# Optimization experiments

Hardware: AMD Instinct MI355X
Metric: run time of the kernel (lower is better)

## Reference

```python
import jax, jax.numpy as jnp
import numpy as np

ICM2IFS = 2.99792458e-05
KB = 0.6950389


def _forward(T, Er, cortim, dt, psi0, Hfull, W1, b1, W2, b2, W3, b3, W4, b4,
             save_interval, remat=False):
    # Faithful vectorized translation of MLNISE.forward with T_correction='ML',
    # explicitTemp='None', saveCoherence=False, saveU=False. The original
    # nested (ii, jj) Python loops are fully independent across (ii, jj), so
    # they are vectorized into one [B, N, N] pass per timestep.
    B, Tp1, N, _ = Hfull.shape
    kBT = T * KB                                             # [B]
    factor = (1j * 2.0 * np.pi * ICM2IFS) * dt.astype(jnp.complex64)  # [B]
    E0, C0 = jnp.linalg.eigh(Hfull[:, 0])
    phiB0 = jnp.einsum('bji,bjk->bik', C0.astype(jnp.complex64),
                       psi0.astype(jnp.complex64))           # Cold^T @ psi0
    jidx = jnp.arange(N)[None, :, None]

    def mlp(x):
        h = jax.nn.elu(x @ W1.T + b1)
        h = jax.nn.elu(h @ W2.T + b2)
        h = jax.nn.elu(h @ W3.T + b3)
        return jax.nn.elu(h @ W4.T + b4)

    def step(carry, Ht):
        Cold, Eold, phiB = carry
        E, C = jnp.linalg.eigh(Ht)
        S = jnp.einsum('bja,bjc->bac', C, Cold)              # S[b, jj, ii] = (C^T Cold)
        kk = jnp.argmax(S * S, axis=1)                       # [B, N] max over jj per ii
        is_kk = jidx == kk[:, None, :]                       # [B, N(jj), N(ii)]
        DE = jnp.where(is_kk, 0.0, E[:, :, None] - Eold[:, None, :])
        phi2 = jnp.real(phiB[:, :, 0]) ** 2 + jnp.imag(phiB[:, :, 0]) ** 2  # [B, N]
        p_ii = phi2[:, None, :]
        p_jj = phi2[:, :, None]
        m = p_ii > 0.01 * p_jj
        ratio = jnp.where(m, p_jj / jnp.where(m, p_ii, 1.0), 100.0)
        kbt = kBT[:, None, None]
        ones = jnp.ones_like(S)
        feat = jnp.stack([DE, ratio, S, kbt * ones,
                          Er[:, None, None] * ones, cortim[:, None, None] * ones,
                          jnp.zeros_like(S), jnp.exp(DE / kbt)], axis=-1)  # [B,N,N,8]
        corr = (mlp(feat.reshape(B * N * N, 8)) + 1.0).reshape(B, N, N)
        S2 = S * corr
        CD = jnp.sum(jnp.where(is_kk, 0.0, S2 * S2), axis=1)  # [B, N] per ii
        S_kk = jnp.take_along_axis(S2, kk[:, None, :], axis=1)[:, 0, :]  # [B, N]
        nrm = jnp.abs(S_kk)
        nrm = jnp.where(nrm > 0, nrm, 1.0)
        pos = (1.0 - CD) > 0
        newval = jnp.where(pos, jnp.sqrt(jnp.clip(1.0 - CD, 0.0)) * S_kk / nrm, S_kk)
        S2 = jnp.where(is_kk, newval[:, None, :], S2)
        phase = jnp.exp(-E.astype(jnp.complex64) * factor[:, None])  # [B, N]
        U = phase[:, :, None] * S2.astype(jnp.complex64)      # diag(phase) @ S
        phiB = U @ phiB
        phiB = phiB / jnp.sqrt(jnp.sum(jnp.real(phiB) ** 2 + jnp.imag(phiB) ** 2,
                                       axis=1, keepdims=True))
        ploc = jnp.einsum('bij,bjk->bik', C.astype(jnp.complex64), phiB)
        ps = jnp.real(ploc[:, :, 0]) ** 2 + jnp.imag(ploc[:, :, 0]) ** 2
        return (C, E, phiB), ps

    f = jax.checkpoint(step) if remat else step
    Hts = jnp.moveaxis(Hfull[:, 1:], 1, 0)                   # time-major [steps,B,N,N]
    _, ps_all = jax.lax.scan(f, (C0, E0, phiB0), Hts)
    saved = jnp.moveaxis(ps_all[save_interval - 1::save_interval], 0, 1)
    return jnp.concatenate([(psi0[:, :, 0] ** 2)[:, None, :], saved], axis=1)


def setup_inputs() -> dict:
    key = jax.random.key(0)
    ks = jax.random.split(key, 8)
    B, N, steps, SI = 32, 32, 600, 10
    A = 50.0 * jax.random.normal(ks[0], (B, steps + 1, N, N), dtype=jnp.float32)
    Hfull = 0.5 * (A + jnp.swapaxes(A, -1, -2))              # symmetric per snapshot
    psi0 = jnp.zeros((B, N, 1), jnp.float32).at[:, 0, 0].set(1.0)
    T = 250.0 + 100.0 * jax.random.uniform(ks[1], (B,), jnp.float32)
    Er = 1.0 + 35.0 * jax.random.uniform(ks[2], (B,), jnp.float32)
    cortim = 10.0 + 100.0 * jax.random.uniform(ks[3], (B,), jnp.float32)
    dt = jnp.ones((B,), jnp.float32)
    total_time = jnp.full((B,), float(steps), jnp.float32)
    reps = jnp.arange(B, dtype=jnp.int32)

    def lin(k, fo, fi):
        kw, kb = jax.random.split(k)
        bnd = 1.0 / np.sqrt(fi)
        W = jax.random.uniform(kw, (fo, fi), jnp.float32, -bnd, bnd) / 10.0
        b = jax.random.uniform(kb, (fo,), jnp.float32, -bnd, bnd)
        return W, b

    W1, b1 = lin(ks[4], 75, 8)
    W2, b2 = lin(ks[5], 75, 75)
    W3, b3 = lin(ks[6], 75, 75)
    W4, b4 = lin(ks[7], 1, 75)
    return dict(T=T, Er=Er, cortim=cortim, total_time=total_time, dt=dt, reps=reps,
                psi0=psi0, Hfull=Hfull, W1=W1, b1=b1, W2=W2, b2=b2, W3=W3, b3=b3,
                W4=W4, b4=b4, save_interval=SI)


def reference(T, Er, cortim, total_time, dt, reps, psi0, Hfull,
              W1, b1, W2, b2, W3, b3, W4, b4, save_interval):
    # total_time/dt only set the (static) number of steps = Hfull.shape[1]-1;
    # reps only sets the batch size. Both are encoded in the array shapes.
    return _forward(T, Er, cortim, dt, psi0, Hfull,
                    W1, b1, W2, b2, W3, b3, W4, b4, save_interval)
```

## Files before the change

kernel.cpp:

```cpp
#include <hip/hip_runtime.h>
#include <math.h>


#define NB 32
#define NN 32
#define NSTEPS 600
#define NT1 601
#define NSI 10
#define NH 75
#define NU 80
#define NKB 20
#define NIB 8
#define NG 16

#define ICM2IFS 2.99792458e-05
#define KBOLTZ 0.6950389f
#define TWO_PI 6.283185307179586476925286766559

__device__ __forceinline__ float elu1(float x) { return x > 0.f ? x : (__expf(x) - 1.f); }

__global__ __launch_bounds__(128) void eigh_kernel(const float* __restrict__ Hf,
                                                   float* __restrict__ E_all,
                                                   float* __restrict__ CT_all)
{
    __shared__ double A[NN][NN + 1];
    __shared__ float  V[NN][NN + 1];
    __shared__ double csC[16], csS[16];
    __shared__ int   prC[16], qrC[16];
    __shared__ double redv;
    __shared__ int   rankl[NN];

    const int idx = blockIdx.x;
    const int tid = threadIdx.x;
    const float* Hp = Hf + (size_t)idx * (NN * NN);

    for (int e = tid; e < NN * NN; e += 128) {
        A[e >> 5][e & 31] = (double)Hp[e];
        V[e >> 5][e & 31] = ((e >> 5) == (e & 31)) ? 1.f : 0.f;
    }
    __syncthreads();

    if (tid < 64) {
        double part = 0.0;
        for (int e = tid; e < NN * NN; e += 64) { double v = A[e >> 5][e & 31]; part += v * v; }
        #pragma unroll
        for (int off = 32; off > 0; off >>= 1) part += __shfl_down(part, off);
        if (tid == 0) redv = part;
    }
    __syncthreads();
    const double tol2 = 1e-16 * redv;

    for (int sweep = 0; sweep < 10; ++sweep) {
        for (int r = 0; r < NN - 1; ++r) {
            if (tid < 16) {
                int m = tid, p, q;
                if (m == 0) { p = 0; q = 1 + (r % 31); }
                else { p = 1 + ((m + r) % 31); q = 1 + ((31 - m + r) % 31); }
                double apq = A[p][q];
                double c = 1.0, sn = 0.0;
                if (apq != 0.0) {
                    double theta = 0.5 * (A[q][q] - A[p][p]) / apq;
                    double tt = 1.0 / (fabs(theta) + sqrt(theta * theta + 1.0));
                    if (theta < 0.0) tt = -tt;
                    c = 1.0 / sqrt(tt * tt + 1.0);
                    sn = tt * c;
                }
                csC[m] = c; csS[m] = sn; prC[m] = p; qrC[m] = q;
            }
            __syncthreads();
            #pragma unroll
            for (int it = 0; it < 4; ++it) {
                int task = tid + it * 128;
                int m = task >> 5, jc = task & 31;
                int p = prC[m], q = qrC[m];
                double c = csC[m], sn = csS[m];
                double ap = A[p][jc], aq = A[q][jc];
                A[p][jc] = c * ap - sn * aq;
                A[q][jc] = sn * ap + c * aq;
            }
            __syncthreads();
            #pragma unroll
            for (int it = 0; it < 8; ++it) {
                int task = tid + it * 128;
                int m = (task >> 5) & 15, ir = task & 31;
                int p = prC[m], q = qrC[m];
                if (task < 512) {
                    double c = csC[m], sn = csS[m];
                    double aip = A[ir][p], aiq = A[ir][q];
                    A[ir][p] = c * aip - sn * aiq;
                    A[ir][q] = sn * aip + c * aiq;
                } else {
                    float cf = (float)csC[m], sf = (float)csS[m];
                    float vip = V[ir][p], viq = V[ir][q];
                    V[ir][p] = cf * vip - sf * viq;
                    V[ir][q] = sf * vip + cf * viq;
                }
            }
            __syncthreads();
        }
        if (sweep >= 3) {
            if (tid < 64) {
                double o = 0.0;
                for (int e = tid; e < NN * NN; e += 64) {
                    int i2 = e >> 5, j2 = e & 31;
                    double v = A[i2][j2];
                    o += (i2 != j2) ? v * v : 0.0;
                }
                #pragma unroll
                for (int off = 32; off > 0; off >>= 1) o += __shfl_down(o, off);
                if (tid == 0) redv = o;
            }
            __syncthreads();
            if (redv <= tol2) break;
        }
    }
    __syncthreads();

    if (tid < NN) {
        double ei = A[tid][tid];
        int rk = 0;
        for (int j2 = 0; j2 < NN; ++j2) {
            double ej = A[j2][j2];
            rk += (ej < ei || (ej == ei && j2 < tid)) ? 1 : 0;
        }
        rankl[tid] = rk;
        E_all[(size_t)idx * NN + rk] = (float)ei;
    }
    __syncthreads();
    float* ct = CT_all + (size_t)idx * NN * NN;
    for (int e = tid; e < NN * NN; e += 128) {
        int col = e >> 5, m2 = e & 31;
        ct[(size_t)rankl[col] * NN + m2] = V[m2][col];
    }
}

__global__ __launch_bounds__(256) void kk_kernel(const float* __restrict__ CT_all,
                                                 int* __restrict__ kk_all)
{
    __shared__ float Ct[NN][NN + 1], Cp[NN][NN + 1], S[NN][NN + 1];
    const int blk = blockIdx.x;
    const int b = blk / NSTEPS, s = blk % NSTEPS + 1;
    const int tid = threadIdx.x;
    const float* ctg = CT_all + ((size_t)b * NT1 + s) * (NN * NN);
    const float* cpg = CT_all + ((size_t)b * NT1 + s - 1) * (NN * NN);
    for (int e = tid; e < NN * NN; e += 256) {
        Ct[e >> 5][e & 31] = ctg[e];
        Cp[e >> 5][e & 31] = cpg[e];
    }
    __syncthreads();
    for (int e = tid; e < NN * NN; e += 256) {
        int i = e >> 5, j = e & 31;
        float acc = 0.f;
        for (int m = 0; m < NN; ++m) acc += Ct[i][m] * Cp[j][m];
        S[i][j] = acc;
    }
    __syncthreads();
    if (tid < NN) {
        const int j = tid;
        float best = -1.f; int bi = 0;
        for (int i = 0; i < NN; ++i) {
            float v = S[i][j]; v *= v;
            if (v > best) { best = v; bi = i; }
        }
        kk_all[(size_t)blk * NN + j] = bi;
    }
}

__global__ void wtrans_kernel(const float* __restrict__ W1, const float* __restrict__ b1,
                              const float* __restrict__ W2, const float* __restrict__ W3,
                              const float* __restrict__ b2, const float* __restrict__ b3,
                              const float* __restrict__ W4,
                              float* __restrict__ W2p, float* __restrict__ W3p,
                              float4* __restrict__ L1W4, float4* __restrict__ L1B4,
                              float* __restrict__ bpad)
{
    const int tid = threadIdx.x;
    const int tot = NG * NKB * 4 * 8;
    for (int e = tid; e < tot; e += 256) {
        int ug = e / (NKB * 4 * 8);
        int kb = (e / (4 * 8)) % NKB;
        int kp = (e / 8) & 3;
        int uu = e & 7;
        int u = ug * 5 + uu;
        int k = kb * 4 + kp;
        float v2 = 0.f, v3 = 0.f;
        if (uu < 5 && u < NH && k < NH) {
            v2 = W2[u * NH + k];
            v3 = W3[u * NH + k];
        }
        W2p[e] = v2; W3p[e] = v3;
    }
    if (tid < NU) {
        if (tid < NH) {
            const float* w = W1 + tid * 8;
            L1W4[tid] = make_float4(w[0], w[1], w[2], w[7]);
            L1B4[tid] = make_float4(w[3], w[4], w[5], b1[tid]);
            bpad[tid]          = b2[tid];
            bpad[NU + tid]     = b3[tid];
            bpad[2 * NU + tid] = W4[tid];
        } else {
            L1W4[tid] = make_float4(0.f, 0.f, 0.f, 0.f);
            L1B4[tid] = make_float4(0.f, 0.f, 0.f, 0.f);
            bpad[tid] = 0.f; bpad[NU + tid] = 0.f; bpad[2 * NU + tid] = 0.f;
        }
    }
}

__global__ __launch_bounds__(1024) void persist_kernel(
    const float* __restrict__ E_all, const float* __restrict__ CT_all,
    const int* __restrict__ kk_all, const float* __restrict__ psi0,
    const float* __restrict__ Tarr, const float* __restrict__ ErA,
    const float* __restrict__ ctA, const float* __restrict__ dtA,
    const float* __restrict__ W2p, const float* __restrict__ W3p,
    const float4* __restrict__ L1W4g, const float4* __restrict__ L1B4g,
    const float* __restrict__ bpad, const float* __restrict__ b4v,
    double* __restrict__ part_g, unsigned int* __restrict__ cnt,
    float* __restrict__ out)
{
    extern __shared__ __align__(16) float dyn[];
    float4* L1Wl = (float4*)dyn;
    float4* L1Bl = L1Wl + NU;
    float* cst  = (float*)(L1Bl + NU);
    float* b2l  = cst + NU;
    float* b3l  = b2l + NU;
    float* W4l  = b3l + NU;
    float* hbuf = W4l + NU;

    __shared__ float CpN[2][NN][NN + 4];
    __shared__ float4 featS[128];
    __shared__ float2 a4b2[NG][64];
    __shared__ float EL[2][NN];
    __shared__ int   kkL[2][NN];
    __shared__ double phre[NN], phim[NN];
    __shared__ double ppre[4][NN], ppim[4][NN];
    __shared__ double sre[NN], sim[NN];
    __shared__ float phi2l[NN];

    const int tid  = threadIdx.x;
    const int b    = blockIdx.x >> 3;
    const int iblk = blockIdx.x & 7;
    const int j0   = iblk * 4;
    const int ug   = __builtin_amdgcn_readfirstlane(tid >> 6);
    const int rg   = tid & 63;
    const int U    = ug * 5;

    const float kbt = KBOLTZ * Tarr[b];
    const float er  = ErA[b];
    const float cti = ctA[b];
    const double dtb = (double)dtA[b];
    const float b4s = b4v[0];

    const float4* W2g = (const float4*)(W2p + (size_t)ug * (NKB * 32));
    const float4* W3g = (const float4*)(W3p + (size_t)ug * (NKB * 32));

    if (tid < NU) {
        L1Wl[tid] = L1W4g[tid];
        L1Bl[tid] = L1B4g[tid];
        b2l[tid] = bpad[tid];
        b3l[tid] = bpad[NU + tid];
        W4l[tid] = bpad[2 * NU + tid];
    }
    __syncthreads();
    if (tid < NU) {
        float4 lb = L1Bl[tid];
        cst[tid] = lb.w + lb.x * kbt + lb.y * er + lb.z * cti;
    }

    {
        const float* c0g = CT_all + (size_t)b * NT1 * NN * NN;
        const float* c1g = c0g + NN * NN;
        for (int e = tid; e < NN * NN; e += 1024) {
            CpN[0][e >> 5][e & 31] = c0g[e];
            CpN[1][e >> 5][e & 31] = c1g[e];
        }
        if (tid < NN) {
            EL[0][tid] = E_all[((size_t)b * NT1 + 0) * NN + tid];
            EL[1][tid] = E_all[((size_t)b * NT1 + 1) * NN + tid];
            kkL[1][tid] = kk_all[(size_t)b * NSTEPS * NN + tid];
        }
        __syncthreads();
        if (tid < NN) {
            const int i = tid;
            double acc = 0.0;
            for (int j = 0; j < NN; ++j) acc += (double)CpN[0][i][j] * (double)psi0[b * NN + j];
            phre[i] = acc; phim[i] = 0.0;
            phi2l[i] = (float)(acc * acc);
            if (iblk == 0) {
                float p0 = psi0[b * NN + i];
                out[((size_t)b * 61) * NN + i] = p0 * p0;
            }
        }
        __syncthreads();
        {
            const int r = tid >> 3, c = tid & 7;
            const int i = r & 31, j = j0 + (r >> 5);
            float Sv = 0.f;
            #pragma unroll
            for (int m = c; m < NN; m += 8)
                Sv += CpN[1][i][m] * CpN[0][j][m];
            Sv += __shfl_xor(Sv, 1); Sv += __shfl_xor(Sv, 2); Sv += __shfl_xor(Sv, 4);
            if (c == 0) {
                const int kj = kkL[1][j];
                const float DE = (i == kj) ? 0.f : (EL[1][i] - EL[0][j]);
                featS[r] = make_float4(DE, 100.f, Sv, __expf(DE / kbt));
            }
        }
        __syncthreads();
        if (tid < 128) {
            const int i = tid & 31, j = j0 + (tid >> 5);
            const float p_i = phi2l[i], p_j = phi2l[j];
            featS[tid].y = (p_j > 0.01f * p_i) ? (p_i / p_j) : 100.f;
        }
    }

    for (int t = 1; t <= NSTEPS; ++t) {
        __syncthreads();
        const int cur = t & 1;

        float2 cpre = make_float2(0.f, 0.f);
        float  epre = 0.f;
        int    kpre = 0;
        if (t < NSTEPS) {
            if (tid < 512) {
                const float* c1g = CT_all + ((size_t)b * NT1 + t + 1) * (NN * NN);
                cpre = ((const float2*)c1g)[tid];
            }
            if (tid < NN) epre = E_all[((size_t)b * NT1 + t + 1) * NN + tid];
            else if (tid < 2 * NN) kpre = kk_all[((size_t)b * NSTEPS + t) * NN + (tid - NN)];
        }

        {
            float4 f0 = featS[2 * rg], f1 = featS[2 * rg + 1];
            #pragma unroll
            for (int u = 0; u < 5; ++u) {
                float4 wv = L1Wl[U + u];
                float c = cst[U + u];
                float2 hv;
                hv.x = elu1(c + wv.x * f0.x + wv.y * f0.y + wv.z * f0.z + wv.w * f0.w);
                hv.y = elu1(c + wv.x * f1.x + wv.y * f1.y + wv.z * f1.z + wv.w * f1.w);
                *(float2*)(hbuf + (U + u) * 128 + 2 * rg) = hv;
            }
        }
        __syncthreads();

        float2 acc[5];
        #pragma unroll
        for (int u = 0; u < 5; ++u) { float bb = b2l[U + u]; acc[u] = make_float2(bb, bb); }
        for (int kb = 0; kb < NKB; ++kb) {
            float4 wv[8];
            float2 hv[4];
            #pragma unroll
            for (int m = 0; m < 8; ++m) wv[m] = W2g[kb * 8 + m];
            #pragma unroll
            for (int kk = 0; kk < 4; ++kk)
                hv[kk] = *(const float2*)(hbuf + (kb * 4 + kk) * 128 + 2 * rg);
            #pragma unroll
            for (int kk = 0; kk < 4; ++kk) {
                const float* wf = (const float*)&wv[kk * 2];
                #pragma unroll
                for (int u = 0; u < 5; ++u) {
                    float wS = wf[u];
                    acc[u].x += wS * hv[kk].x; acc[u].y += wS * hv[kk].y;
                }
            }
        }
        __syncthreads();
        #pragma unroll
        for (int u = 0; u < 5; ++u) {
            float2 hv; hv.x = elu1(acc[u].x); hv.y = elu1(acc[u].y);
            *(float2*)(hbuf + (U + u) * 128 + 2 * rg) = hv;
        }
        __syncthreads();

        #pragma unroll
        for (int u = 0; u < 5; ++u) { float bb = b3l[U + u]; acc[u] = make_float2(bb, bb); }
        for (int kb = 0; kb < NKB; ++kb) {
            float4 wv[8];
            float2 hv[4];
            #pragma unroll
            for (int m = 0; m < 8; ++m) wv[m] = W3g[kb * 8 + m];
            #pragma unroll
            for (int kk = 0; kk < 4; ++kk)
                hv[kk] = *(const float2*)(hbuf + (kb * 4 + kk) * 128 + 2 * rg);
            #pragma unroll
            for (int kk = 0; kk < 4; ++kk) {
                const float* wf = (const float*)&wv[kk * 2];
                #pragma unroll
                for (int u = 0; u < 5; ++u) {
                    float wS = wf[u];
                    acc[u].x += wS * hv[kk].x; acc[u].y += wS * hv[kk].y;
                }
            }
        }
        {
            float2 p4 = make_float2(0.f, 0.f);
            #pragma unroll
            for (int u = 0; u < 5; ++u) {
                float w4 = W4l[U + u];
                p4.x += w4 * elu1(acc[u].x); p4.y += w4 * elu1(acc[u].y);
            }
            a4b2[ug][rg] = p4;
        }
        __syncthreads();

        if (tid < 128) {
            const int r = tid;
            const int i = r & 31;
            const int jj = r >> 5;
            const int j = j0 + jj;
            float a4 = b4s;
            #pragma unroll
            for (int g = 0; g < NG; ++g) {
                float2 pv = a4b2[g][r >> 1];
                a4 += (r & 1) ? pv.y : pv.x;
            }
            const float corr = elu1(a4) + 1.f;
            float s2v = featS[r].z * corr;
            const int kj = kkL[cur][j];
            double v = (double)s2v;
            double cd = (i == kj) ? 0.0 : v * v;
            cd += __shfl_xor(cd, 1);  cd += __shfl_xor(cd, 2);
            cd += __shfl_xor(cd, 4);  cd += __shfl_xor(cd, 8);
            cd += __shfl_xor(cd, 16);
            if (i == kj) {
                double nrm = fabs(v); nrm = (nrm > 0.0) ? nrm : 1.0;
                double rem = 1.0 - cd;
                v = (rem > 0.0) ? (sqrt(rem) * v / nrm) : v;
                v = (double)(float)v;
            }
            ppre[jj][i] = v * phre[j];
            ppim[jj][i] = v * phim[j];
        }

        if (t < NSTEPS) {
            if (tid < 512) {
                const int e0 = tid * 2;
                CpN[1 - cur][e0 >> 5][e0 & 31] = cpre.x;
                CpN[1 - cur][e0 >> 5][(e0 & 31) + 1] = cpre.y;
            }
            if (tid < NN) EL[1 - cur][tid] = epre;
            else if (tid < 2 * NN) kkL[1 - cur][tid - NN] = kpre;
        }
        __syncthreads();

        if (tid < 32) {
            const int i = tid;
            double pr = ((ppre[0][i] + ppre[1][i]) + ppre[2][i]) + ppre[3][i];
            double pi = ((ppim[0][i] + ppim[1][i]) + ppim[2][i]) + ppim[3][i];
            double* pg = part_g + ((size_t)cur * NB + b) * 512;
            __hip_atomic_store(&pg[i * 8 + iblk], pr,
                               __ATOMIC_RELAXED, __HIP_MEMORY_SCOPE_AGENT);
            __hip_atomic_store(&pg[256 + i * 8 + iblk], pi,
                               __ATOMIC_RELAXED, __HIP_MEMORY_SCOPE_AGENT);
            asm volatile("s_waitcnt vmcnt(0)" ::: "memory");
            if (tid == 0)
                __hip_atomic_fetch_add(cnt + (size_t)b * NSTEPS + (t - 1), 1u,
                                       __ATOMIC_RELAXED, __HIP_MEMORY_SCOPE_AGENT);
        }

        if (t < NSTEPS) {
            const int curS = 1 - cur;
            const int r = tid >> 3, c = tid & 7;
            const int i = r & 31, j = j0 + (r >> 5);
            float Sv = 0.f;
            #pragma unroll
            for (int m = c; m < NN; m += 8)
                Sv += CpN[curS][i][m] * CpN[1 - curS][j][m];
            Sv += __shfl_xor(Sv, 1); Sv += __shfl_xor(Sv, 2); Sv += __shfl_xor(Sv, 4);
            if (c == 0) {
                const int kj = kkL[curS][j];
                const float DE = (i == kj) ? 0.f : (EL[curS][i] - EL[1 - curS][j]);
                featS[r] = make_float4(DE, 100.f, Sv, __expf(DE / kbt));
            }
        }

        if (tid == 0) {
            const unsigned int* c = cnt + (size_t)b * NSTEPS + (t - 1);
            while (__hip_atomic_load(c, __ATOMIC_RELAXED, __HIP_MEMORY_SCOPE_AGENT)
                   < (unsigned)NIB) {
                __builtin_amdgcn_s_sleep(2);
            }
        }
        __syncthreads();

        if (tid < 512) {
            const double* pg = part_g + ((size_t)cur * NB + b) * 512;
            double v = __hip_atomic_load(&pg[tid], __ATOMIC_RELAXED,
                                         __HIP_MEMORY_SCOPE_AGENT);
            v += __shfl_xor(v, 1); v += __shfl_xor(v, 2); v += __shfl_xor(v, 4);
            if ((tid & 7) == 0) {
                const int i = (tid >> 3) & 31;
                if (tid < 256) sre[i] = v; else sim[i] = v;
            }
        }
        __syncthreads();

        if (tid < NN) {
            const int ii = tid;
            double are = sre[ii], aim = sim[ii];
            double th = (double)EL[cur][ii] * (TWO_PI * ICM2IFS) * dtb;
            double x2 = th * th;
            double sph = th * (1.0 + x2 * (-1.0 / 6.0 + x2 * (1.0 / 120.0 + x2 * (-1.0 / 5040.0 + x2 * (1.0 / 362880.0)))));
            double cph = 1.0 + x2 * (-0.5 + x2 * (1.0 / 24.0 + x2 * (-1.0 / 720.0 + x2 * (1.0 / 40320.0))));
            double nre = cph * are + sph * aim;
            double nim = cph * aim - sph * are;
            double v = nre * nre + nim * nim;
            double s = v;
            s += __shfl_xor(s, 1); s += __shfl_xor(s, 2); s += __shfl_xor(s, 4);
            s += __shfl_xor(s, 8); s += __shfl_xor(s, 16);
            double sc = 1.0 / sqrt(s);
            double nr = nre * sc, ni = nim * sc;
            phre[ii] = nr; phim[ii] = ni;
            phi2l[ii] = (float)(nr * nr + ni * ni);
        }
        __syncthreads();

        if ((t % NSI) == 0 && tid < 64) {
            const int ii = iblk * 4 + (tid >> 4), l = tid & 15;
            double are = 0.0, aim = 0.0;
            #pragma unroll
            for (int jj = l; jj < NN; jj += 16) {
                double cij = (double)CpN[cur][jj][ii];
                are += cij * phre[jj]; aim += cij * phim[jj];
            }
            are += __shfl_xor(are, 1); aim += __shfl_xor(aim, 1);
            are += __shfl_xor(are, 2); aim += __shfl_xor(aim, 2);
            are += __shfl_xor(are, 4); aim += __shfl_xor(aim, 4);
            are += __shfl_xor(are, 8); aim += __shfl_xor(aim, 8);
            if (l == 0)
                out[((size_t)b * 61 + t / NSI) * NN + ii] = (float)(are * are + aim * aim);
        }
        if (t < NSTEPS && tid < 128) {
            const int i = tid & 31, j = j0 + (tid >> 5);
            const float p_i = phi2l[i], p_j = phi2l[j];
            featS[tid].y = (p_j > 0.01f * p_i) ? (p_i / p_j) : 100.f;
        }
    }
}

extern "C" void kernel_launch(void* const* d_in, const int* in_sizes, int n_in,
                              void* d_out, int out_size, void* d_ws, size_t ws_size,
                              hipStream_t stream)
{
    const float* Tarr = (const float*)d_in[0];
    const float* ErA  = (const float*)d_in[1];
    const float* ctA  = (const float*)d_in[2];
    const float* dtA  = (const float*)d_in[4];
    const float* psi0 = (const float*)d_in[6];
    const float* Hf   = (const float*)d_in[7];
    const float* W1   = (const float*)d_in[8];
    const float* b1   = (const float*)d_in[9];
    const float* W2   = (const float*)d_in[10];
    const float* b2   = (const float*)d_in[11];
    const float* W3   = (const float*)d_in[12];
    const float* b3   = (const float*)d_in[13];
    const float* W4   = (const float*)d_in[14];
    const float* b4   = (const float*)d_in[15];

    unsigned int* cnt = (unsigned int*)d_ws;
    float* E_all  = (float*)(cnt + (size_t)NB * NSTEPS);
    float* CT_all = E_all + (size_t)NB * NT1 * NN;
    float* W2p    = CT_all + (size_t)NB * NT1 * NN * NN;
    float* W3p    = W2p + NG * NKB * 32;
    float4* L1W4  = (float4*)(W3p + NG * NKB * 32);
    float4* L1B4  = L1W4 + NU;
    float* bpad   = (float*)(L1B4 + NU);
    double* part_g = (double*)(bpad + 3 * NU);
    int*   kk_all = (int*)(part_g + 2 * (size_t)NB * 512);
    float* outp   = (float*)d_out;

    hipMemsetAsync(cnt, 0, (size_t)NB * NSTEPS * sizeof(unsigned int), stream);
    eigh_kernel<<<NB * NT1, 128, 0, stream>>>(Hf, E_all, CT_all);
    wtrans_kernel<<<1, 256, 0, stream>>>(W1, b1, W2, W3, b2, b3, W4,
                                         W2p, W3p, L1W4, L1B4, bpad);
    kk_kernel<<<NB * NSTEPS, 256, 0, stream>>>(CT_all, kk_all);

    const size_t dynf = (size_t)(8 * NU) + 4 * NU + NU * 128;
    persist_kernel<<<NB * NIB, 1024, dynf * sizeof(float), stream>>>(E_all, CT_all,
        kk_all, psi0, Tarr, ErA, ctA, dtA, W2p, W3p, L1W4, L1B4, bpad, b4,
        part_g, cnt, outp);
}
```

Measured before the change: 12.37 ms.

## Use one wavefront per Jacobi eigensolve and trim per-step barriers in persistent kernel

The Jacobi eigensolver now handles two matrices per block, one per 64-lane wavefront. Rotation coefficients move between lanes by shuffles instead of shared memory, and block-wide __syncthreads are replaced by wave barriers. In the persistent time-step kernel, the population-ratio feature is computed inline in the MLP input load, which removes a separate pass and its barrier. The cross-block partial-sum layout is transposed so that one wave reads and sums the eight partials and does the phase rotation and normalisation without extra block barriers. The trade-off is more work per lane in the eigensolver, and correctness now depends on wave-level LDS ordering via s_waitcnt.

```diff
diff --git a/kernel.cpp b/kernel.cpp
--- a/kernel.cpp
+++ b/kernel.cpp
@@ -23,114 +23,110 @@
                                                    float* __restrict__ E_all,
                                                    float* __restrict__ CT_all)
 {
-    __shared__ double A[NN][NN + 1];
-    __shared__ float  V[NN][NN + 1];
-    __shared__ double csC[16], csS[16];
-    __shared__ int   prC[16], qrC[16];
-    __shared__ double redv;
-    __shared__ int   rankl[NN];
-
-    const int idx = blockIdx.x;
-    const int tid = threadIdx.x;
+    __shared__ double A[2][NN][NN + 1];
+    __shared__ float  V[2][NN][NN + 1];
+    __shared__ int    rankl[2][NN];
+
+    const int w    = threadIdx.x >> 6;
+    const int lane = threadIdx.x & 63;
+    const int idx  = blockIdx.x * 2 + w;
     const float* Hp = Hf + (size_t)idx * (NN * NN);
-
-    for (int e = tid; e < NN * NN; e += 128) {
-        A[e >> 5][e & 31] = (double)Hp[e];
-        V[e >> 5][e & 31] = ((e >> 5) == (e & 31)) ? 1.f : 0.f;
-    }
-    __syncthreads();
-
-    if (tid < 64) {
-        double part = 0.0;
-        for (int e = tid; e < NN * NN; e += 64) { double v = A[e >> 5][e & 31]; part += v * v; }
-        #pragma unroll
-        for (int off = 32; off > 0; off >>= 1) part += __shfl_down(part, off);
-        if (tid == 0) redv = part;
-    }
-    __syncthreads();
-    const double tol2 = 1e-16 * redv;
+    double (*Aw)[NN + 1] = A[w];
+    float  (*Vw)[NN + 1] = V[w];
+
+    for (int e = lane; e < NN * NN; e += 64) {
+        Aw[e >> 5][e & 31] = (double)Hp[e];
+        Vw[e >> 5][e & 31] = ((e >> 5) == (e & 31)) ? 1.f : 0.f;
+    }
+    asm volatile("s_waitcnt lgkmcnt(0)" ::: "memory");
+    __builtin_amdgcn_wave_barrier();
+
+    double part = 0.0;
+    for (int e = lane; e < NN * NN; e += 64) { double v = Aw[e >> 5][e & 31]; part += v * v; }
+    #pragma unroll
+    for (int off = 32; off > 0; off >>= 1) part += __shfl_down(part, off);
+    const double tol2 = 1e-16 * __shfl(part, 0);
 
     for (int sweep = 0; sweep < 10; ++sweep) {
         for (int r = 0; r < NN - 1; ++r) {
-            if (tid < 16) {
-                int m = tid, p, q;
+            double cR = 1.0, sR = 0.0;
+            if (lane < 16) {
+                int m = lane, p, q;
                 if (m == 0) { p = 0; q = 1 + (r % 31); }
                 else { p = 1 + ((m + r) % 31); q = 1 + ((31 - m + r) % 31); }
-                double apq = A[p][q];
-                double c = 1.0, sn = 0.0;
+                double apq = Aw[p][q];
                 if (apq != 0.0) {
-                    double theta = 0.5 * (A[q][q] - A[p][p]) / apq;
+                    double theta = 0.5 * (Aw[q][q] - Aw[p][p]) / apq;
                     double tt = 1.0 / (fabs(theta) + sqrt(theta * theta + 1.0));
                     if (theta < 0.0) tt = -tt;
-                    c = 1.0 / sqrt(tt * tt + 1.0);
-                    sn = tt * c;
+                    cR = 1.0 / sqrt(tt * tt + 1.0);
+                    sR = tt * cR;
                 }
-                csC[m] = c; csS[m] = sn; prC[m] = p; qrC[m] = q;
-            }
-            __syncthreads();
-            #pragma unroll
-            for (int it = 0; it < 4; ++it) {
-                int task = tid + it * 128;
+            }
+            __builtin_amdgcn_wave_barrier();
+            #pragma unroll
+            for (int it = 0; it < 8; ++it) {
+                int task = lane + it * 64;
                 int m = task >> 5, jc = task & 31;
-                int p = prC[m], q = qrC[m];
-                double c = csC[m], sn = csS[m];
-                double ap = A[p][jc], aq = A[q][jc];
-                A[p][jc] = c * ap - sn * aq;
-                A[q][jc] = sn * ap + c * aq;
-            }
-            __syncthreads();
-            #pragma unroll
-            for (int it = 0; it < 8; ++it) {
-                int task = tid + it * 128;
+                int p = (m == 0) ? 0 : 1 + ((m + r) % 31);
+                int q = (m == 0) ? 1 + (r % 31) : 1 + ((31 - m + r) % 31);
+                double c = __shfl(cR, m), sn = __shfl(sR, m);
+                double ap = Aw[p][jc], aq = Aw[q][jc];
+                Aw[p][jc] = c * ap - sn * aq;
+                Aw[q][jc] = sn * ap + c * aq;
+            }
+            asm volatile("s_waitcnt lgkmcnt(0)" ::: "memory");
+            __builtin_amdgcn_wave_barrier();
+            #pragma unroll
+            for (int it = 0; it < 16; ++it) {
+                int task = lane + it * 64;
                 int m = (task >> 5) & 15, ir = task & 31;
-                int p = prC[m], q = qrC[m];
+                int p = (m == 0) ? 0 : 1 + ((m + r) % 31);
+                int q = (m == 0) ? 1 + (r % 31) : 1 + ((31 - m + r) % 31);
+                double c = __shfl(cR, m), sn = __shfl(sR, m);
                 if (task < 512) {
-                    double c = csC[m], sn = csS[m];
-                    double aip = A[ir][p], aiq = A[ir][q];
-                    A[ir][p] = c * aip - sn * aiq;
-                    A[ir][q] = sn * aip + c * aiq;
+                    double aip = Aw[ir][p], aiq = Aw[ir][q];
+                    Aw[ir][p] = c * aip - sn * aiq;
+                    Aw[ir][q] = sn * aip + c * aiq;
                 } else {
-                    float cf = (float)csC[m], sf = (float)csS[m];
-                    float vip = V[ir][p], viq = V[ir][q];
-                    V[ir][p] = cf * vip - sf * viq;
-                    V[ir][q] = sf * vip + cf * viq;
+                    float cf = (float)c, sf = (float)sn;
+                    float vip = Vw[ir][p], viq = Vw[ir][q];
+                    Vw[ir][p] = cf * vip - sf * viq;
+                    Vw[ir][q] = sf * vip + cf * viq;
                 }
             }
-            __syncthreads();
+            asm volatile("s_waitcnt lgkmcnt(0)" ::: "memory");
+            __builtin_amdgcn_wave_barrier();
         }
         if (sweep >= 3) {
-            if (tid < 64) {
-                double o = 0.0;
-                for (int e = tid; e < NN * NN; e += 64) {
-                    int i2 = e >> 5, j2 = e & 31;
-                    double v = A[i2][j2];
-                    o += (i2 != j2) ? v * v : 0.0;
-                }
-                #pragma unroll
-                for (int off = 32; off > 0; off >>= 1) o += __shfl_down(o, off);
-                if (tid == 0) redv = o;
-            }
-            __syncthreads();
-            if (redv <= tol2) break;
-        }
-    }
-    __syncthreads();
-
-    if (tid < NN) {
-        double ei = A[tid][tid];
+            double o = 0.0;
+            for (int e = lane; e < NN * NN; e += 64) {
+                int i2 = e >> 5, j2 = e & 31;
+                double v = Aw[i2][j2];
+                o += (i2 != j2) ? v * v : 0.0;
+            }
+            #pragma unroll
+            for (int off = 32; off > 0; off >>= 1) o += __shfl_down(o, off);
+            if (__shfl(o, 0) <= tol2) break;
+        }
+    }
+
+    if (lane < NN) {
+        double ei = Aw[lane][lane];
         int rk = 0;
         for (int j2 = 0; j2 < NN; ++j2) {
-            double ej = A[j2][j2];
-            rk += (ej < ei || (ej == ei && j2 < tid)) ? 1 : 0;
-        }
-        rankl[tid] = rk;
+            double ej = Aw[j2][j2];
+            rk += (ej < ei || (ej == ei && j2 < lane)) ? 1 : 0;
+        }
+        rankl[w][lane] = rk;
         E_all[(size_t)idx * NN + rk] = (float)ei;
     }
-    __syncthreads();
+    asm volatile("s_waitcnt lgkmcnt(0)" ::: "memory");
+    __builtin_amdgcn_wave_barrier();
     float* ct = CT_all + (size_t)idx * NN * NN;
-    for (int e = tid; e < NN * NN; e += 128) {
+    for (int e = lane; e < NN * NN; e += 64) {
         int col = e >> 5, m2 = e & 31;
-        ct[(size_t)rankl[col] * NN + m2] = V[m2][col];
+        ct[(size_t)rankl[w][col] * NN + m2] = Vw[m2][col];
     }
 }
 
@@ -233,7 +229,6 @@
     __shared__ int   kkL[2][NN];
     __shared__ double phre[NN], phim[NN];
     __shared__ double ppre[4][NN], ppim[4][NN];
-    __shared__ double sre[NN], sim[NN];
     __shared__ float phi2l[NN];
 
     const int tid  = threadIdx.x;
@@ -305,12 +300,6 @@
                 featS[r] = make_float4(DE, 100.f, Sv, __expf(DE / kbt));
             }
         }
-        __syncthreads();
-        if (tid < 128) {
-            const int i = tid & 31, j = j0 + (tid >> 5);
-            const float p_i = phi2l[i], p_j = phi2l[j];
-            featS[tid].y = (p_j > 0.01f * p_i) ? (p_i / p_j) : 100.f;
-        }
     }
 
     for (int t = 1; t <= NSTEPS; ++t) {
@@ -331,6 +320,12 @@
 
         {
             float4 f0 = featS[2 * rg], f1 = featS[2 * rg + 1];
+            const int jc  = j0 + (rg >> 4);
+            const int ic0 = (2 * rg) & 31;
+            const float pj  = phi2l[jc];
+            const float pi0 = phi2l[ic0], pi1 = phi2l[ic0 + 1];
+            f0.y = (pj > 0.01f * pi0) ? (pi0 / pj) : 100.f;
+            f1.y = (pj > 0.01f * pi1) ? (pi1 / pj) : 100.f;
             #pragma unroll
             for (int u = 0; u < 5; ++u) {
                 float4 wv = L1Wl[U + u];
@@ -448,9 +443,9 @@
             double pr = ((ppre[0][i] + ppre[1][i]) + ppre[2][i]) + ppre[3][i];
             double pi = ((ppim[0][i] + ppim[1][i]) + ppim[2][i]) + ppim[3][i];
             double* pg = part_g + ((size_t)cur * NB + b) * 512;
-            __hip_atomic_store(&pg[i * 8 + iblk], pr,
+            __hip_atomic_store(&pg[iblk * 32 + i], pr,
                                __ATOMIC_RELAXED, __HIP_MEMORY_SCOPE_AGENT);
-            __hip_atomic_store(&pg[256 + i * 8 + iblk], pi,
+            __hip_atomic_store(&pg[256 + iblk * 32 + i], pi,
                                __ATOMIC_RELAXED, __HIP_MEMORY_SCOPE_AGENT);
             asm volatile("s_waitcnt vmcnt(0)" ::: "memory");
             if (tid == 0)
@@ -483,57 +478,53 @@
         }
         __syncthreads();
 
-        if (tid < 512) {
-            const double* pg = part_g + ((size_t)cur * NB + b) * 512;
-            double v = __hip_atomic_load(&pg[tid], __ATOMIC_RELAXED,
-                                         __HIP_MEMORY_SCOPE_AGENT);
-            v += __shfl_xor(v, 1); v += __shfl_xor(v, 2); v += __shfl_xor(v, 4);
-            if ((tid & 7) == 0) {
-                const int i = (tid >> 3) & 31;
-                if (tid < 256) sre[i] = v; else sim[i] = v;
-            }
-        }
-        __syncthreads();
-
-        if (tid < NN) {
-            const int ii = tid;
-            double are = sre[ii], aim = sim[ii];
-            double th = (double)EL[cur][ii] * (TWO_PI * ICM2IFS) * dtb;
-            double x2 = th * th;
-            double sph = th * (1.0 + x2 * (-1.0 / 6.0 + x2 * (1.0 / 120.0 + x2 * (-1.0 / 5040.0 + x2 * (1.0 / 362880.0)))));
-            double cph = 1.0 + x2 * (-0.5 + x2 * (1.0 / 24.0 + x2 * (-1.0 / 720.0 + x2 * (1.0 / 40320.0))));
-            double nre = cph * are + sph * aim;
-            double nim = cph * aim - sph * are;
-            double v = nre * nre + nim * nim;
-            double s = v;
-            s += __shfl_xor(s, 1); s += __shfl_xor(s, 2); s += __shfl_xor(s, 4);
-            s += __shfl_xor(s, 8); s += __shfl_xor(s, 16);
-            double sc = 1.0 / sqrt(s);
-            double nr = nre * sc, ni = nim * sc;
-            phre[ii] = nr; phim[ii] = ni;
-            phi2l[ii] = (float)(nr * nr + ni * ni);
-        }
-        __syncthreads();
-
-        if ((t % NSI) == 0 && tid < 64) {
-            const int ii = iblk * 4 + (tid >> 4), l = tid & 15;
-            double are = 0.0, aim = 0.0;
-            #pragma unroll
-            for (int jj = l; jj < NN; jj += 16) {
-                double cij = (double)CpN[cur][jj][ii];
-                are += cij * phre[jj]; aim += cij * phim[jj];
-            }
-            are += __shfl_xor(are, 1); aim += __shfl_xor(aim, 1);
-            are += __shfl_xor(are, 2); aim += __shfl_xor(aim, 2);
-            are += __shfl_xor(are, 4); aim += __shfl_xor(aim, 4);
-            are += __shfl_xor(are, 8); aim += __shfl_xor(aim, 8);
-            if (l == 0)
-                out[((size_t)b * 61 + t / NSI) * NN + ii] = (float)(are * are + aim * aim);
-        }
-        if (t < NSTEPS && tid < 128) {
-            const int i = tid & 31, j = j0 + (tid >> 5);
-            const float p_i = phi2l[i], p_j = phi2l[j];
-            featS[tid].y = (p_j > 0.01f * p_i) ? (p_i / p_j) : 100.f;
+        if (tid < 64) {
+            const int comp = tid >> 5, i2 = tid & 31;
+            const double* pg = part_g + ((size_t)cur * NB + b) * 512 + comp * 256;
+            double v0 = __hip_atomic_load(&pg[0 * 32 + i2], __ATOMIC_RELAXED, __HIP_MEMORY_SCOPE_AGENT);
+            double v1 = __hip_atomic_load(&pg[1 * 32 + i2], __ATOMIC_RELAXED, __HIP_MEMORY_SCOPE_AGENT);
+            double v2 = __hip_atomic_load(&pg[2 * 32 + i2], __ATOMIC_RELAXED, __HIP_MEMORY_SCOPE_AGENT);
+            double v3 = __hip_atomic_load(&pg[3 * 32 + i2], __ATOMIC_RELAXED, __HIP_MEMORY_SCOPE_AGENT);
+            double v4 = __hip_atomic_load(&pg[4 * 32 + i2], __ATOMIC_RELAXED, __HIP_MEMORY_SCOPE_AGENT);
+            double v5 = __hip_atomic_load(&pg[5 * 32 + i2], __ATOMIC_RELAXED, __HIP_MEMORY_SCOPE_AGENT);
+            double v6 = __hip_atomic_load(&pg[6 * 32 + i2], __ATOMIC_RELAXED, __HIP_MEMORY_SCOPE_AGENT);
+            double v7 = __hip_atomic_load(&pg[7 * 32 + i2], __ATOMIC_RELAXED, __HIP_MEMORY_SCOPE_AGENT);
+            double tot = ((v0 + v1) + (v2 + v3)) + ((v4 + v5) + (v6 + v7));
+            double oth = __shfl_xor(tot, 32);
+            if (tid < 32) {
+                double are = tot, aim = oth;
+                double th = (double)EL[cur][i2] * (TWO_PI * ICM2IFS) * dtb;
+                double x2 = th * th;
+                double sph = th * (1.0 + x2 * (-1.0 / 6.0 + x2 * (1.0 / 120.0 + x2 * (-1.0 / 5040.0 + x2 * (1.0 / 362880.0)))));
+                double cph = 1.0 + x2 * (-0.5 + x2 * (1.0 / 24.0 + x2 * (-1.0 / 720.0 + x2 * (1.0 / 40320.0))));
+                double nre = cph * are + sph * aim;
+                double nim = cph * aim - sph * are;
+                double vv = nre * nre + nim * nim;
+                double s = vv;
+                s += __shfl_xor(s, 1); s += __shfl_xor(s, 2); s += __shfl_xor(s, 4);
+                s += __shfl_xor(s, 8); s += __shfl_xor(s, 16);
+                double sc2 = 1.0 / sqrt(s);
+                double nr = nre * sc2, ni = nim * sc2;
+                phre[i2] = nr; phim[i2] = ni;
+                phi2l[i2] = (float)(nr * nr + ni * ni);
+            }
+            asm volatile("s_waitcnt lgkmcnt(0)" ::: "memory");
+            __builtin_amdgcn_wave_barrier();
+            if ((t % NSI) == 0) {
+                const int ii = iblk * 4 + (tid >> 4), l = tid & 15;
+                double are = 0.0, aim = 0.0;
+                #pragma unroll
+                for (int jj = l; jj < NN; jj += 16) {
+                    double cij = (double)CpN[cur][jj][ii];
+                    are += cij * phre[jj]; aim += cij * phim[jj];
+                }
+                are += __shfl_xor(are, 1); aim += __shfl_xor(aim, 1);
+                are += __shfl_xor(are, 2); aim += __shfl_xor(aim, 2);
+                are += __shfl_xor(are, 4); aim += __shfl_xor(aim, 4);
+                are += __shfl_xor(are, 8); aim += __shfl_xor(aim, 8);
+                if (l == 0)
+                    out[((size_t)b * 61 + t / NSI) * NN + ii] = (float)(are * are + aim * aim);
+            }
         }
     }
 }
@@ -570,7 +561,7 @@
     float* outp   = (float*)d_out;
 
     hipMemsetAsync(cnt, 0, (size_t)NB * NSTEPS * sizeof(unsigned int), stream);
-    eigh_kernel<<<NB * NT1, 128, 0, stream>>>(Hf, E_all, CT_all);
+    eigh_kernel<<<NB * NT1 / 2, 128, 0, stream>>>(Hf, E_all, CT_all);
     wtrans_kernel<<<1, 256, 0, stream>>>(W1, b1, W2, W3, b2, b3, W4,
                                          W2p, W3p, L1W4, L1B4, bpad);
     kk_kernel<<<NB * NSTEPS, 256, 0, stream>>>(CT_all, kk_all);
```

Measured after the change: 15.06 ms. 21.8% more time.

## Fuse argmax overlap computation into persistent kernel and drop kk_kernel

Applied to the files above, without the earlier changes.

Removes the separate kk_kernel launch that computed the per-column argmax of the squared overlap matrix for every step and stored it to global memory. Each persistent block now recomputes the overlap column for its own j slice and reduces the argmax with warp shuffles, then fills DE and exp(DE/kbt) into the features. This work runs on otherwise idle threads (256-383) alongside the phase-update threads. It saves a kernel launch and global traffic at the cost of redundant dot products and a serial 32-term loop per thread inside the critical per-step path. Tie-breaking changes slightly to lowest index on equal values.

```diff
diff --git a/kernel.cpp b/kernel.cpp
--- a/kernel.cpp
+++ b/kernel.cpp
@@ -131,38 +131,6 @@
     for (int e = tid; e < NN * NN; e += 128) {
         int col = e >> 5, m2 = e & 31;
         ct[(size_t)rankl[col] * NN + m2] = V[m2][col];
-    }
-}
-
-__global__ __launch_bounds__(256) void kk_kernel(const float* __restrict__ CT_all,
-                                                 int* __restrict__ kk_all)
-{
-    __shared__ float Ct[NN][NN + 1], Cp[NN][NN + 1], S[NN][NN + 1];
-    const int blk = blockIdx.x;
-    const int b = blk / NSTEPS, s = blk % NSTEPS + 1;
-    const int tid = threadIdx.x;
-    const float* ctg = CT_all + ((size_t)b * NT1 + s) * (NN * NN);
-    const float* cpg = CT_all + ((size_t)b * NT1 + s - 1) * (NN * NN);
-    for (int e = tid; e < NN * NN; e += 256) {
-        Ct[e >> 5][e & 31] = ctg[e];
-        Cp[e >> 5][e & 31] = cpg[e];
-    }
-    __syncthreads();
-    for (int e = tid; e < NN * NN; e += 256) {
-        int i = e >> 5, j = e & 31;
-        float acc = 0.f;
-        for (int m = 0; m < NN; ++m) acc += Ct[i][m] * Cp[j][m];
-        S[i][j] = acc;
-    }
-    __syncthreads();
-    if (tid < NN) {
-        const int j = tid;
-        float best = -1.f; int bi = 0;
-        for (int i = 0; i < NN; ++i) {
-            float v = S[i][j]; v *= v;
-            if (v > best) { best = v; bi = i; }
-        }
-        kk_all[(size_t)blk * NN + j] = bi;
     }
 }
 
@@ -208,7 +176,7 @@
 
 __global__ __launch_bounds__(1024) void persist_kernel(
     const float* __restrict__ E_all, const float* __restrict__ CT_all,
-    const int* __restrict__ kk_all, const float* __restrict__ psi0,
+    const float* __restrict__ psi0,
     const float* __restrict__ Tarr, const float* __restrict__ ErA,
     const float* __restrict__ ctA, const float* __restrict__ dtA,
     const float* __restrict__ W2p, const float* __restrict__ W3p,
@@ -276,7 +244,6 @@
         if (tid < NN) {
             EL[0][tid] = E_all[((size_t)b * NT1 + 0) * NN + tid];
             EL[1][tid] = E_all[((size_t)b * NT1 + 1) * NN + tid];
-            kkL[1][tid] = kk_all[(size_t)b * NSTEPS * NN + tid];
         }
         __syncthreads();
         if (tid < NN) {
@@ -299,17 +266,29 @@
             for (int m = c; m < NN; m += 8)
                 Sv += CpN[1][i][m] * CpN[0][j][m];
             Sv += __shfl_xor(Sv, 1); Sv += __shfl_xor(Sv, 2); Sv += __shfl_xor(Sv, 4);
-            if (c == 0) {
-                const int kj = kkL[1][j];
-                const float DE = (i == kj) ? 0.f : (EL[1][i] - EL[0][j]);
-                featS[r] = make_float4(DE, 100.f, Sv, __expf(DE / kbt));
-            }
+            if (c == 0) featS[r] = make_float4(0.f, 0.f, Sv, 0.f);
         }
         __syncthreads();
         if (tid < 128) {
-            const int i = tid & 31, j = j0 + (tid >> 5);
+            const int r = tid, i = r & 31;
+            const int j = j0 + (r >> 5);
+            float svq = 0.f;
+            for (int m = 0; m < NN; ++m)
+                svq += CpN[1][i][m] * CpN[0][j][m];
+            float v2 = svq * svq;
+            int bi = i;
+            #pragma unroll
+            for (int off = 16; off > 0; off >>= 1) {
+                float ov = __shfl_xor(v2, off);
+                int   oi = __shfl_xor(bi, off);
+                if (ov > v2 || (ov == v2 && oi < bi)) { v2 = ov; bi = oi; }
+            }
+            if (i == 0) kkL[1][j] = bi;
+            const float DE = (i == bi) ? 0.f : (EL[1][i] - EL[0][j]);
+            const float Sv = featS[r].z;
             const float p_i = phi2l[i], p_j = phi2l[j];
-            featS[tid].y = (p_j > 0.01f * p_i) ? (p_i / p_j) : 100.f;
+            const float ratio = (p_j > 0.01f * p_i) ? (p_i / p_j) : 100.f;
+            featS[r] = make_float4(DE, ratio, Sv, __expf(DE / kbt));
         }
     }
 
@@ -319,14 +298,12 @@
 
         float2 cpre = make_float2(0.f, 0.f);
         float  epre = 0.f;
-        int    kpre = 0;
         if (t < NSTEPS) {
             if (tid < 512) {
                 const float* c1g = CT_all + ((size_t)b * NT1 + t + 1) * (NN * NN);
                 cpre = ((const float2*)c1g)[tid];
             }
             if (tid < NN) epre = E_all[((size_t)b * NT1 + t + 1) * NN + tid];
-            else if (tid < 2 * NN) kpre = kk_all[((size_t)b * NSTEPS + t) * NN + (tid - NN)];
         }
 
         {
@@ -439,7 +416,6 @@
                 CpN[1 - cur][e0 >> 5][(e0 & 31) + 1] = cpre.y;
             }
             if (tid < NN) EL[1 - cur][tid] = epre;
-            else if (tid < 2 * NN) kkL[1 - cur][tid - NN] = kpre;
         }
         __syncthreads();
 
@@ -467,11 +443,7 @@
             for (int m = c; m < NN; m += 8)
                 Sv += CpN[curS][i][m] * CpN[1 - curS][j][m];
             Sv += __shfl_xor(Sv, 1); Sv += __shfl_xor(Sv, 2); Sv += __shfl_xor(Sv, 4);
-            if (c == 0) {
-                const int kj = kkL[curS][j];
-                const float DE = (i == kj) ? 0.f : (EL[curS][i] - EL[1 - curS][j]);
-                featS[r] = make_float4(DE, 100.f, Sv, __expf(DE / kbt));
-            }
+            if (c == 0) featS[r] = make_float4(0.f, 0.f, Sv, 0.f);
         }
 
         if (tid == 0) {
@@ -512,6 +484,26 @@
             double nr = nre * sc, ni = nim * sc;
             phre[ii] = nr; phim[ii] = ni;
             phi2l[ii] = (float)(nr * nr + ni * ni);
+        } else if (t < NSTEPS && tid >= 256 && tid < 384) {
+            const int r = tid - 256;
+            const int i = r & 31;
+            const int j = j0 + (r >> 5);
+            const int curS = 1 - cur;
+            float svq = 0.f;
+            for (int m = 0; m < NN; ++m)
+                svq += CpN[curS][i][m] * CpN[cur][j][m];
+            float v2 = svq * svq;
+            int bi = i;
+            #pragma unroll
+            for (int off = 16; off > 0; off >>= 1) {
+                float ov = __shfl_xor(v2, off);
+                int   oi = __shfl_xor(bi, off);
+                if (ov > v2 || (ov == v2 && oi < bi)) { v2 = ov; bi = oi; }
+            }
+            if (i == 0) kkL[curS][j] = bi;
+            const float DE = (i == bi) ? 0.f : (EL[curS][i] - EL[cur][j]);
+            featS[r].x = DE;
+            featS[r].w = __expf(DE / kbt);
         }
         __syncthreads();
 
@@ -566,17 +558,15 @@
     float4* L1B4  = L1W4 + NU;
     float* bpad   = (float*)(L1B4 + NU);
     double* part_g = (double*)(bpad + 3 * NU);
-    int*   kk_all = (int*)(part_g + 2 * (size_t)NB * 512);
     float* outp   = (float*)d_out;
 
     hipMemsetAsync(cnt, 0, (size_t)NB * NSTEPS * sizeof(unsigned int), stream);
     eigh_kernel<<<NB * NT1, 128, 0, stream>>>(Hf, E_all, CT_all);
     wtrans_kernel<<<1, 256, 0, stream>>>(W1, b1, W2, W3, b2, b3, W4,
                                          W2p, W3p, L1W4, L1B4, bpad);
-    kk_kernel<<<NB * NSTEPS, 256, 0, stream>>>(CT_all, kk_all);
 
     const size_t dynf = (size_t)(8 * NU) + 4 * NU + NU * 128;
     persist_kernel<<<NB * NIB, 1024, dynf * sizeof(float), stream>>>(E_all, CT_all,
-        kk_all, psi0, Tarr, ErA, ctA, dtA, W2p, W3p, L1W4, L1B4, bpad, b4,
+        psi0, Tarr, ErA, ctA, dtA, W2p, W3p, L1W4, L1B4, bpad, b4,
         part_g, cnt, outp);
 }
```

Result: no change. 12.42 ms (+0.4%).
